# Performance work log

Measured on AMD Instinct MI355X. Metric: run time of the kernel, lower is better.

Reference implementation:

```python
import jax, jax.numpy as jnp
import numpy as np

# SelectiveAttention (keras) reference.
# - A single shared InputDense (D -> key_dim) projects query, key, value.
# - ComponentBuilder yields (filter_input=Q, context_input=banded K^T, _input=V):
#   scores = (Q K^T / sqrt(key_dim)) masked to the band |i-j| <= band_size
#   (the layer's Softmax sublayer is built but never invoked in call()).
# - attended = scores @ V, then OutputDense (key_dim -> D). Dropout inactive at inference.

def setup_inputs() -> dict:
    key = jax.random.key(0)
    ks = jax.random.split(key, 5)
    B, S, D, Dk = 4, 4096, 512, 64
    query = jax.random.normal(ks[0], (B, S, D), dtype=jnp.float32)
    value = jax.random.normal(ks[1], (B, S, D), dtype=jnp.float32)
    Wi = jax.random.normal(ks[2], (D, Dk), dtype=jnp.float32) * (1.0 / np.sqrt(D))
    bi = jnp.zeros((Dk,), dtype=jnp.float32)
    Wo = jax.random.normal(ks[3], (Dk, D), dtype=jnp.float32) * (1.0 / np.sqrt(Dk))
    bo = jnp.zeros((D,), dtype=jnp.float32)
    return {"query": query, "value": value, "Wi": Wi, "bi": bi,
            "Wo": Wo, "bo": bo, "band_size": 128}


def reference(query, value, Wi, bi, Wo, bo, band_size):
    Dk = Wi.shape[1]
    scale = 1.0 / jnp.sqrt(jnp.asarray(Dk, dtype=query.dtype))
    # shared input projection (same dense for q, k, v; key defaults to value)
    q = query @ Wi + bi            # [B,S,Dk]
    kv = value @ Wi + bi           # [B,S,Dk]  (k == v here)
    scores = jnp.einsum('bqd,bkd->bqk', q, kv) * scale  # [B,S,S]
    S = q.shape[1]
    idx = jnp.arange(S)
    band = (jnp.abs(idx[:, None] - idx[None, :]) <= band_size)  # [S,S] bool
    scores = jnp.where(band[None], scores, 0.0)
    attended = jnp.einsum('bqk,bkd->bqd', scores, kv)    # [B,S,Dk]
    return attended @ Wo + bo                            # [B,S,D]
```

## Files before the change

kernel.cpp:

```cpp
#include <hip/hip_runtime.h>
#include <math.h>


typedef __bf16 bf16;
using bf16x4  = __attribute__((ext_vector_type(4))) __bf16;
using bf16x8  = __attribute__((ext_vector_type(8))) __bf16;
using floatx4 = __attribute__((ext_vector_type(4))) float;

#define MFMA(a, b, c) __builtin_amdgcn_mfma_f32_16x16x32_bf16(a, b, c, 0, 0, 0)

__global__ __launch_bounds__(256) void prep_weights(
    const float* __restrict__ Wi, const float* __restrict__ Wo,
    bf16* __restrict__ WiT, bf16* __restrict__ WoT)
{
    __shared__ float T[64][65];
    const int blk = blockIdx.x, tid = threadIdx.x;
    if (blk < 8) {
        const int k0 = blk * 64;
        #pragma unroll
        for (int i = 0; i < 4; i++) {
            int idx4 = tid * 4 + i;
            int r = idx4 >> 4, c4 = (idx4 & 15) * 4;
            float4 f = *(const float4*)(Wi + (size_t)(k0 + r) * 64 + c4);
            T[r][c4 + 0] = f.x; T[r][c4 + 1] = f.y;
            T[r][c4 + 2] = f.z; T[r][c4 + 3] = f.w;
        }
        __syncthreads();
        #pragma unroll
        for (int i = 0; i < 2; i++) {
            int seg = tid * 2 + i;
            int n = seg >> 3, k8 = (seg & 7) * 8;
            bf16x8 v;
            #pragma unroll
            for (int j = 0; j < 8; j++) v[j] = (bf16)T[k8 + j][n];
            *(bf16x8*)(WiT + (size_t)n * 512 + k0 + k8) = v;
        }
    } else {
        const int n0 = (blk - 8) * 64;
        #pragma unroll
        for (int i = 0; i < 4; i++) {
            int idx4 = tid * 4 + i;
            int r = idx4 >> 4, c4 = (idx4 & 15) * 4;
            float4 f = *(const float4*)(Wo + (size_t)r * 512 + n0 + c4);
            T[r][c4 + 0] = f.x; T[r][c4 + 1] = f.y;
            T[r][c4 + 2] = f.z; T[r][c4 + 3] = f.w;
        }
        __syncthreads();
        #pragma unroll
        for (int i = 0; i < 2; i++) {
            int seg = tid * 2 + i;
            int n = seg >> 3, k8 = (seg & 7) * 8;
            bf16x8 v;
            #pragma unroll
            for (int j = 0; j < 8; j++) v[j] = (bf16)T[k8 + j][n];
            *(bf16x8*)(WoT + (size_t)(n0 + n) * 64 + k8) = v;
        }
    }
}

__global__ __launch_bounds__(256) void proj_in_kernel(
    const float* __restrict__ q, const float* __restrict__ v,
    const bf16* __restrict__ WiT, const float* __restrict__ bi,
    bf16* __restrict__ qp, bf16* __restrict__ kvp, bf16* __restrict__ kvT,
    int K, int S, float scale)
{
    const float* x = blockIdx.z ? v : q;
    bf16* y = blockIdx.z ? kvp : qp;
    const float sc = blockIdx.z ? 1.0f : scale;
    __shared__ float P[4][16][68];
    const int tid = threadIdx.x;
    const int wave = tid >> 6, lane = tid & 63;
    const int lr = lane & 15, lq = lane >> 4;
    const int row0 = blockIdx.x * 16;
    const float* xrow = x + (size_t)(row0 + lr) * K + wave * 128;
    const bf16* wrow = WiT + wave * 128;

    floatx4 acc[4] = {};
    #pragma unroll
    for (int ks = 0; ks < 4; ks++) {
        const int k0 = ks * 32 + lq * 8;
        float4 a0 = *(const float4*)(xrow + k0);
        float4 a1 = *(const float4*)(xrow + k0 + 4);
        bf16x8 af;
        af[0] = (bf16)a0.x; af[1] = (bf16)a0.y; af[2] = (bf16)a0.z; af[3] = (bf16)a0.w;
        af[4] = (bf16)a1.x; af[5] = (bf16)a1.y; af[6] = (bf16)a1.z; af[7] = (bf16)a1.w;
        #pragma unroll
        for (int t = 0; t < 4; t++) {
            bf16x8 bfv = *(const bf16x8*)(wrow + (size_t)(t * 16 + lr) * K + k0);
            acc[t] = MFMA(af, bfv, acc[t]);
        }
    }
    #pragma unroll
    for (int t = 0; t < 4; t++)
        #pragma unroll
        for (int r = 0; r < 4; r++)
            P[wave][lq * 4 + r][t * 16 + lr] = acc[t][r];
    __syncthreads();

    {
        const int row = tid >> 4, c4 = (tid & 15) * 4;
        float4 s0 = *(const float4*)&P[0][row][c4];
        float4 s1 = *(const float4*)&P[1][row][c4];
        float4 s2 = *(const float4*)&P[2][row][c4];
        float4 s3 = *(const float4*)&P[3][row][c4];
        float4 bb = *(const float4*)(bi + c4);
        bf16x4 o;
        o[0] = (bf16)((s0.x + s1.x + s2.x + s3.x + bb.x) * sc);
        o[1] = (bf16)((s0.y + s1.y + s2.y + s3.y + bb.y) * sc);
        o[2] = (bf16)((s0.z + s1.z + s2.z + s3.z + bb.z) * sc);
        o[3] = (bf16)((s0.w + s1.w + s2.w + s3.w + bb.w) * sc);
        *(bf16x4*)(y + (size_t)(row0 + row) * 64 + c4) = o;
    }
    if (blockIdx.z) {
        const int d = tid >> 2, s4 = (tid & 3) * 4;
        const int b = row0 >> 12, s0r = row0 & (S - 1);
        const float bb = bi[d];
        bf16x4 o;
        #pragma unroll
        for (int i = 0; i < 4; i++) {
            float s = P[0][s4 + i][d] + P[1][s4 + i][d]
                    + P[2][s4 + i][d] + P[3][s4 + i][d] + bb;
            o[i] = (bf16)s;
        }
        *(bf16x4*)(kvT + ((size_t)b * 64 + d) * S + s0r + s4) = o;
    }
}

__global__ __launch_bounds__(256) void band_attn_out_kernel(
    const bf16* __restrict__ qp, const bf16* __restrict__ kvp,
    const bf16* __restrict__ kvT, const int* __restrict__ band_ptr,
    const bf16* __restrict__ WoT, const float* __restrict__ bo,
    float* __restrict__ out, int S)
{
    __shared__ bf16 Ss[4][16][88];
    __shared__ float P[4][16][68];
    __shared__ bf16 St[16][72];
    const int tid = threadIdx.x;
    const int wave = tid >> 6, lane = tid & 63;
    const int lr = lane & 15, lq = lane >> 4;
    const int gs = blockIdx.x;
    const int b = gs >> 8;
    const int q0 = (gs & 255) * 16;
    const int band = band_ptr[0];

    const bf16* qb = qp + ((size_t)b * S + q0) * 64;
    bf16x8 qf0 = *(const bf16x8*)(qb + lr * 64 + lq * 8);
    bf16x8 qf1 = *(const bf16x8*)(qb + lr * 64 + 32 + lq * 8);

    floatx4 acc[4] = {};
    const int ch_lo = (q0 - band) >> 6;
    #pragma unroll
    for (int pass = 0; pass < 2; pass++) {
        const int cc = wave + pass * 4;
        if (cc <= 4) {
            const int kj0 = (ch_lo + cc) * 64;
            floatx4 sc[4] = {};
            #pragma unroll
            for (int t = 0; t < 4; t++) {
                int kr = kj0 + t * 16 + lr;
                int krc = min(max(kr, 0), S - 1);
                const bf16* kp = kvp + ((size_t)b * S + krc) * 64;
                bf16x8 b0 = *(const bf16x8*)(kp + lq * 8);
                bf16x8 b1 = *(const bf16x8*)(kp + 32 + lq * 8);
                sc[t] = MFMA(qf0, b0, sc[t]);
                sc[t] = MFMA(qf1, b1, sc[t]);
            }
            #pragma unroll
            for (int t = 0; t < 4; t++) {
                int kj = kj0 + t * 16 + lr;
                bool kv_ok = (kj >= 0) && (kj < S);
                #pragma unroll
                for (int r = 0; r < 4; r++) {
                    int qi = q0 + lq * 4 + r;
                    int dlt = qi - kj; dlt = dlt < 0 ? -dlt : dlt;
                    float vv = (kv_ok && dlt <= band) ? sc[t][r] : 0.f;
                    Ss[wave][lq * 4 + r][t * 16 + lr] = (bf16)vv;
                }
            }
            #pragma unroll
            for (int ks = 0; ks < 2; ks++) {
                bf16x8 sa = *(const bf16x8*)(&Ss[wave][lr][ks * 32 + lq * 8]);
                int kb = kj0 + ks * 32 + lq * 8;
                int kbc = min(max(kb, 0), S - 8);
                #pragma unroll
                for (int t = 0; t < 4; t++) {
                    bf16x8 vb = *(const bf16x8*)(kvT + ((size_t)b * 64 + t * 16 + lr) * S + kbc);
                    acc[t] = MFMA(sa, vb, acc[t]);
                }
            }
        }
    }
    #pragma unroll
    for (int t = 0; t < 4; t++)
        #pragma unroll
        for (int r = 0; r < 4; r++)
            P[wave][lq * 4 + r][t * 16 + lr] = acc[t][r];
    __syncthreads();

    {
        const int row = tid >> 4, c4 = (tid & 15) * 4;
        float4 s0 = *(const float4*)&P[0][row][c4];
        float4 s1 = *(const float4*)&P[1][row][c4];
        float4 s2 = *(const float4*)&P[2][row][c4];
        float4 s3 = *(const float4*)&P[3][row][c4];
        bf16x4 o;
        o[0] = (bf16)(s0.x + s1.x + s2.x + s3.x);
        o[1] = (bf16)(s0.y + s1.y + s2.y + s3.y);
        o[2] = (bf16)(s0.z + s1.z + s2.z + s3.z);
        o[3] = (bf16)(s0.w + s1.w + s2.w + s3.w);
        *(bf16x4*)(&St[row][c4]) = o;
    }
    __syncthreads();

    bf16x8 af0 = *(const bf16x8*)(&St[lr][lq * 8]);
    bf16x8 af1 = *(const bf16x8*)(&St[lr][32 + lq * 8]);
    float* orow = out + ((size_t)b * S + q0) * 512;
    #pragma unroll
    for (int i = 0; i < 8; i++) {
        const int tp = wave * 8 + i;
        const bf16* wp = WoT + (size_t)(tp * 16 + lr) * 64;
        bf16x8 b0 = *(const bf16x8*)(wp + lq * 8);
        bf16x8 b1 = *(const bf16x8*)(wp + 32 + lq * 8);
        floatx4 o = {};
        o = MFMA(af0, b0, o);
        o = MFMA(af1, b1, o);
        float bb = bo[tp * 16 + lr];
        #pragma unroll
        for (int r = 0; r < 4; r++)
            orow[(size_t)(lq * 4 + r) * 512 + tp * 16 + lr] = o[r] + bb;
    }
}

extern "C" void kernel_launch(void* const* d_in, const int* in_sizes, int n_in,
                              void* d_out, int out_size, void* d_ws, size_t ws_size,
                              hipStream_t stream) {
    const float* query = (const float*)d_in[0];
    const float* value = (const float*)d_in[1];
    const float* Wi    = (const float*)d_in[2];
    const float* bi    = (const float*)d_in[3];
    const float* Wo    = (const float*)d_in[4];
    const float* bo    = (const float*)d_in[5];
    const int*   band  = (const int*)d_in[6];
    float* out = (float*)d_out;

    const int Dk = in_sizes[3];
    const int D  = in_sizes[5];
    const int S  = 4096;
    const int BS = in_sizes[0] / D;
    const int B  = BS / S;
    const float scale = 1.0f / sqrtf((float)Dk);

    bf16* WiT = (bf16*)d_ws;
    bf16* WoT = WiT + 32768;
    bf16* qp  = WoT + 32768;
    bf16* kvp = qp  + (size_t)BS * 64;
    bf16* kvT = kvp + (size_t)BS * 64;

    prep_weights<<<16, 256, 0, stream>>>(Wi, Wo, WiT, WoT);

    proj_in_kernel<<<dim3(BS / 16, 1, 2), 256, 0, stream>>>(
        query, value, WiT, bi, qp, kvp, kvT, D, S, scale);

    band_attn_out_kernel<<<dim3(BS / 16), 256, 0, stream>>>(
        qp, kvp, kvT, band, WoT, bo, out, S);
}
```

Before: 146.2 us.

## Fuse query projection into band attention kernel, drop qp intermediate

Moves the Q = query@Wi projection out of the input projection kernel and into the start of the band attention kernel. Each attention block computes its 16 query rows with MFMA, reduces the partial sums through shared memory, scales them, stages them in shared memory and loads the Q fragments from there. The projection kernel now handles only value/kv, so its grid halves and the bf16 qp round trip through global memory disappears. In exchange the attention kernel does more work and needs two extra block barriers before the attention loop, and St is widened to 88 columns.

```diff
diff --git a/kernel.cpp b/kernel.cpp
--- a/kernel.cpp
+++ b/kernel.cpp
@@ -59,20 +59,16 @@
 }
 
 __global__ __launch_bounds__(256) void proj_in_kernel(
-    const float* __restrict__ q, const float* __restrict__ v,
-    const bf16* __restrict__ WiT, const float* __restrict__ bi,
-    bf16* __restrict__ qp, bf16* __restrict__ kvp, bf16* __restrict__ kvT,
-    int K, int S, float scale)
+    const float* __restrict__ v, const bf16* __restrict__ WiT,
+    const float* __restrict__ bi, bf16* __restrict__ kvp,
+    bf16* __restrict__ kvT, int K, int S)
 {
-    const float* x = blockIdx.z ? v : q;
-    bf16* y = blockIdx.z ? kvp : qp;
-    const float sc = blockIdx.z ? 1.0f : scale;
     __shared__ float P[4][16][68];
     const int tid = threadIdx.x;
     const int wave = tid >> 6, lane = tid & 63;
     const int lr = lane & 15, lq = lane >> 4;
     const int row0 = blockIdx.x * 16;
-    const float* xrow = x + (size_t)(row0 + lr) * K + wave * 128;
+    const float* xrow = v + (size_t)(row0 + lr) * K + wave * 128;
     const bf16* wrow = WiT + wave * 128;
 
     floatx4 acc[4] = {};
@@ -105,13 +101,13 @@
         float4 s3 = *(const float4*)&P[3][row][c4];
         float4 bb = *(const float4*)(bi + c4);
         bf16x4 o;
-        o[0] = (bf16)((s0.x + s1.x + s2.x + s3.x + bb.x) * sc);
-        o[1] = (bf16)((s0.y + s1.y + s2.y + s3.y + bb.y) * sc);
-        o[2] = (bf16)((s0.z + s1.z + s2.z + s3.z + bb.z) * sc);
-        o[3] = (bf16)((s0.w + s1.w + s2.w + s3.w + bb.w) * sc);
-        *(bf16x4*)(y + (size_t)(row0 + row) * 64 + c4) = o;
-    }
-    if (blockIdx.z) {
+        o[0] = (bf16)(s0.x + s1.x + s2.x + s3.x + bb.x);
+        o[1] = (bf16)(s0.y + s1.y + s2.y + s3.y + bb.y);
+        o[2] = (bf16)(s0.z + s1.z + s2.z + s3.z + bb.z);
+        o[3] = (bf16)(s0.w + s1.w + s2.w + s3.w + bb.w);
+        *(bf16x4*)(kvp + (size_t)(row0 + row) * 64 + c4) = o;
+    }
+    {
         const int d = tid >> 2, s4 = (tid & 3) * 4;
         const int b = row0 >> 12, s0r = row0 & (S - 1);
         const float bb = bi[d];
@@ -127,14 +123,15 @@
 }
 
 __global__ __launch_bounds__(256) void band_attn_out_kernel(
-    const bf16* __restrict__ qp, const bf16* __restrict__ kvp,
+    const float* __restrict__ query, const bf16* __restrict__ WiT,
+    const float* __restrict__ bi, const bf16* __restrict__ kvp,
     const bf16* __restrict__ kvT, const int* __restrict__ band_ptr,
     const bf16* __restrict__ WoT, const float* __restrict__ bo,
-    float* __restrict__ out, int S)
+    float* __restrict__ out, int K, int S, float scale)
 {
     __shared__ bf16 Ss[4][16][88];
     __shared__ float P[4][16][68];
-    __shared__ bf16 St[16][72];
+    __shared__ bf16 St[16][88];
     const int tid = threadIdx.x;
     const int wave = tid >> 6, lane = tid & 63;
     const int lr = lane & 15, lq = lane >> 4;
@@ -143,9 +140,48 @@
     const int q0 = (gs & 255) * 16;
     const int band = band_ptr[0];
 
-    const bf16* qb = qp + ((size_t)b * S + q0) * 64;
-    bf16x8 qf0 = *(const bf16x8*)(qb + lr * 64 + lq * 8);
-    bf16x8 qf1 = *(const bf16x8*)(qb + lr * 64 + 32 + lq * 8);
+    {
+        const float* xrow = query + ((size_t)b * S + q0 + lr) * K + wave * 128;
+        const bf16* wrow = WiT + wave * 128;
+        floatx4 qa[4] = {};
+        #pragma unroll
+        for (int ks = 0; ks < 4; ks++) {
+            const int k0 = ks * 32 + lq * 8;
+            float4 a0 = *(const float4*)(xrow + k0);
+            float4 a1 = *(const float4*)(xrow + k0 + 4);
+            bf16x8 af;
+            af[0] = (bf16)a0.x; af[1] = (bf16)a0.y; af[2] = (bf16)a0.z; af[3] = (bf16)a0.w;
+            af[4] = (bf16)a1.x; af[5] = (bf16)a1.y; af[6] = (bf16)a1.z; af[7] = (bf16)a1.w;
+            #pragma unroll
+            for (int t = 0; t < 4; t++) {
+                bf16x8 bfv = *(const bf16x8*)(wrow + (size_t)(t * 16 + lr) * K + k0);
+                qa[t] = MFMA(af, bfv, qa[t]);
+            }
+        }
+        #pragma unroll
+        for (int t = 0; t < 4; t++)
+            #pragma unroll
+            for (int r = 0; r < 4; r++)
+                P[wave][lq * 4 + r][t * 16 + lr] = qa[t][r];
+    }
+    __syncthreads();
+    {
+        const int row = tid >> 4, c4 = (tid & 15) * 4;
+        float4 s0 = *(const float4*)&P[0][row][c4];
+        float4 s1 = *(const float4*)&P[1][row][c4];
+        float4 s2 = *(const float4*)&P[2][row][c4];
+        float4 s3 = *(const float4*)&P[3][row][c4];
+        float4 bb = *(const float4*)(bi + c4);
+        bf16x4 o;
+        o[0] = (bf16)((s0.x + s1.x + s2.x + s3.x + bb.x) * scale);
+        o[1] = (bf16)((s0.y + s1.y + s2.y + s3.y + bb.y) * scale);
+        o[2] = (bf16)((s0.z + s1.z + s2.z + s3.z + bb.z) * scale);
+        o[3] = (bf16)((s0.w + s1.w + s2.w + s3.w + bb.w) * scale);
+        *(bf16x4*)(&St[row][c4]) = o;
+    }
+    __syncthreads();
+    bf16x8 qf0 = *(const bf16x8*)(&St[lr][lq * 8]);
+    bf16x8 qf1 = *(const bf16x8*)(&St[lr][32 + lq * 8]);
 
     floatx4 acc[4] = {};
     const int ch_lo = (q0 - band) >> 6;
@@ -252,15 +288,14 @@
 
     bf16* WiT = (bf16*)d_ws;
     bf16* WoT = WiT + 32768;
-    bf16* qp  = WoT + 32768;
-    bf16* kvp = qp  + (size_t)BS * 64;
+    bf16* kvp = WoT + 32768;
     bf16* kvT = kvp + (size_t)BS * 64;
 
     prep_weights<<<16, 256, 0, stream>>>(Wi, Wo, WiT, WoT);
 
-    proj_in_kernel<<<dim3(BS / 16, 1, 2), 256, 0, stream>>>(
-        query, value, WiT, bi, qp, kvp, kvT, D, S, scale);
+    proj_in_kernel<<<dim3(BS / 16), 256, 0, stream>>>(
+        value, WiT, bi, kvp, kvT, D, S);
 
     band_attn_out_kernel<<<dim3(BS / 16), 256, 0, stream>>>(
-        qp, kvp, kvT, band, WoT, bo, out, S);
+        query, WiT, bi, kvp, kvT, band, WoT, bo, out, D, S, scale);
 }
```

Result: no change. 145.8 us (-0.3%).
